# Kernel tuning notes

Hardware: AMD Instinct MI355X
Metric: run time of the kernel (lower is better)

## Reference

```python
import jax, jax.numpy as jnp
import numpy as np

NUM_LAYERS = 3
CHANNELS = 8
IN_CHANNELS = 8
MASK_OUT_STRIDE = 4
WEIGHT_NUMS = [(IN_CHANNELS + 2) * CHANNELS, CHANNELS * CHANNELS, CHANNELS]  # [80, 64, 8]
BIAS_NUMS = [CHANNELS, CHANNELS, 1]
NUM_GEN = sum(WEIGHT_NUMS) + sum(BIAS_NUMS)  # 169


def parse_params(params, weight_nums, bias_nums, channels):
    # params: [n_inst, sum(weight_nums)+sum(bias_nums)]
    n = params.shape[0]
    sizes = list(weight_nums) + list(bias_nums)
    splits = jnp.split(params, np.cumsum(sizes)[:-1].tolist(), axis=1)
    L = len(weight_nums)
    ws, bs = [], []
    for l in range(L):
        cout = channels if l < L - 1 else 1
        ws.append(splits[l].reshape(n, cout, -1))       # [n, cout, cin]
        bs.append(splits[L + l].reshape(n, cout))        # [n, cout]
    return ws, bs


def mask_head(x, ws, bs):
    # x: [n, cin, HW]; per-instance 1x1 convs == batched small GEMMs
    x_concat = None
    L = len(ws)
    for i, (w, b) in enumerate(zip(ws, bs)):
        x = jnp.einsum('noc,nch->noh', w, x) + b[:, :, None]
        if i < L - 1:
            x = jax.nn.relu(x)
        if i == L - 2:
            x_concat = x
    return x, x_concat


def aligned_bilinear(x, factor):
    # faithful port of AdelaiDet aligned_bilinear (align_corners=True interp)
    if factor == 1:
        return x
    n, c, h, w = x.shape
    x = jnp.pad(x, ((0, 0), (0, 0), (0, 1), (0, 1)), mode='edge')  # [h+1, w+1]
    oh, ow = factor * h + 1, factor * w + 1

    def interp_axis(arr, out_len, axis):
        # align_corners=True with out = factor*in - factor + 1 -> src = dst/factor exactly
        pos = jnp.arange(out_len) / factor
        i0 = jnp.floor(pos).astype(jnp.int32)
        i1 = jnp.minimum(i0 + 1, arr.shape[axis] - 1)
        frac = (pos - i0).astype(arr.dtype)
        a0 = jnp.take(arr, i0, axis=axis)
        a1 = jnp.take(arr, i1, axis=axis)
        shp = [1] * arr.ndim
        shp[axis] = out_len
        frac = frac.reshape(shp)
        return a0 * (1 - frac) + a1 * frac

    x = interp_axis(x, oh, 2)
    x = interp_axis(x, ow, 3)
    p = factor // 2
    x = jnp.pad(x, ((0, 0), (0, 0), (p, 0), (p, 0)), mode='edge')
    return x[:, :, :oh - 1, :ow - 1]


def setup_inputs() -> dict:
    key = jax.random.key(0)
    k1, k2, k3, k4, k5, k6 = jax.random.split(key, 6)
    N, Cin, H, W = 2, IN_CHANNELS, 100, 152
    n_inst = 128
    return {
        'mask_feats_body': jax.random.normal(k1, (N, Cin, H, W), dtype=jnp.float32),
        'mask_feats_edge': jax.random.normal(k2, (N, Cin, H, W), dtype=jnp.float32),
        'mask_head_params': jax.random.normal(k3, (n_inst, 2 * NUM_GEN + 81), dtype=jnp.float32) * 0.2,
        'inst_locations': jax.random.uniform(k4, (n_inst, 2), dtype=jnp.float32) * jnp.array([W * 8.0, H * 8.0]),
        'sizes_of_interest': jnp.array([64.0, 128.0, 256.0, 512.0, 1024.0], dtype=jnp.float32),
        'im_inds': jax.random.randint(k5, (n_inst,), 0, N, dtype=jnp.int32),
        'fpn_levels': jax.random.randint(k6, (n_inst,), 0, 5, dtype=jnp.int32),
        'mask_feat_stride': 8,
    }


def reference(mask_feats_body, mask_feats_edge, mask_head_params, inst_locations,
              sizes_of_interest, im_inds, fpn_levels, mask_feat_stride):
    N, Cin, H, W = mask_feats_body.shape
    n_inst = mask_head_params.shape[0]
    stride = mask_feat_stride

    # compute_locations: (x, y) grid at feature stride, offset stride//2
    shifts_x = jnp.arange(W, dtype=jnp.float32) * stride + stride // 2
    shifts_y = jnp.arange(H, dtype=jnp.float32) * stride + stride // 2
    sy, sx = jnp.meshgrid(shifts_y, shifts_x, indexing='ij')
    locations = jnp.stack([sx.reshape(-1), sy.reshape(-1)], axis=1)  # [HW, 2]

    rel = inst_locations[:, None, :] - locations[None, :, :]          # [n, HW, 2]
    rel = jnp.transpose(rel, (0, 2, 1))                               # [n, 2, HW]
    soi = sizes_of_interest[fpn_levels]                               # [n]
    rel = rel / soi[:, None, None]

    fb = mask_feats_body[im_inds].reshape(n_inst, Cin, H * W)
    fe = mask_feats_edge[im_inds].reshape(n_inst, Cin, H * W)
    inp_b = jnp.concatenate([rel, fb], axis=1)   # [n, Cin+2, HW]
    inp_e = jnp.concatenate([rel, fe], axis=1)

    wb, bb = parse_params(mask_head_params[:, :NUM_GEN], WEIGHT_NUMS, BIAS_NUMS, CHANNELS)
    we, be = parse_params(mask_head_params[:, NUM_GEN:2 * NUM_GEN], WEIGHT_NUMS, BIAS_NUMS, CHANNELS)
    wf, bf = parse_params(mask_head_params[:, 2 * NUM_GEN:], WEIGHT_NUMS[1:], BIAS_NUMS[1:], CHANNELS)

    logits_b, concat_b = mask_head(inp_b, wb, bb)
    logits_e, concat_e = mask_head(inp_e, we, be)
    logits_f, _ = mask_head(concat_b + concat_e, wf, bf)

    factor = mask_feat_stride // MASK_OUT_STRIDE
    outs = []
    for l in (logits_b, logits_e, logits_f):
        l = l.reshape(n_inst, 1, H, W)
        outs.append(jax.nn.sigmoid(aligned_bilinear(l, factor)))
    return tuple(outs)
```

## Files before the change

kernel.cpp:

```cpp
#include <hip/hip_runtime.h>
#include <hip/hip_bf16.h>
#include <hip/hip_fp16.h>

#define CIN      8
#define HH       100
#define WW       152
#define HWSZ     (HH * WW)
#define OHGT     200
#define OWID     304
#define PPI      419
#define OUT_PER_INST (OHGT * OWID)

#define RSTRIP   5
#define TROWS    6
#define NSTRIPS  20
#define QPT      38
#define P1THREADS (TROWS * QPT)
#define P2ITEMS  (3 * RSTRIP * 76)


typedef float vf4 __attribute__((ext_vector_type(4)));

__device__ __forceinline__ vf4 fma4(float w, vf4 x, vf4 a) { return w * x + a; }
__device__ __forceinline__ vf4 relu4(vf4 x) {
    vf4 r; r.x = fmaxf(x.x, 0.f); r.y = fmaxf(x.y, 0.f);
    r.z = fmaxf(x.z, 0.f); r.w = fmaxf(x.w, 0.f); return r;
}

__global__ __launch_bounds__(256, 4) void dmh_fused6_kernel(
    const float* __restrict__ fbody,
    const float* __restrict__ fedge,
    const float* __restrict__ params,
    const float* __restrict__ locs,
    const float* __restrict__ soi_tab,
    const int*   __restrict__ im_inds,
    const int*   __restrict__ fpn_levels,
    float* __restrict__ out,
    int n_inst)
{
    const int s   = blockIdx.x;
    const int n   = blockIdx.y;
    const int tid = threadIdx.x;
    const int r0  = RSTRIP * s;

    __shared__ float slog[3][TROWS][WW];

    const float* __restrict__ p = params + (size_t)n * PPI;
    const int   im      = im_inds[n];
    const float inv_soi = 1.0f / soi_tab[fpn_levels[n]];
    const float sx = (locs[2 * n]     - 4.0f) * inv_soi;
    const float sy = (locs[2 * n + 1] - 4.0f) * inv_soi;
    const float k8 = 8.0f * inv_soi;

    if (tid < P1THREADS) {
        const int rl = tid / QPT;
        const int c  = (tid - rl * QPT) * 4;
        const int r  = min(r0 + rl, HH - 1);
        const int px = r * WW + c;

        const float dx0 = sx - (float)c * k8;
        const vf4 dx = { dx0, dx0 - k8, dx0 - 2.f * k8, dx0 - 3.f * k8 };
        const float dyv = sy - (float)r * k8;
        const vf4 dy = { dyv, dyv, dyv, dyv };

        const float* __restrict__ fb = fbody + (size_t)im * CIN * HWSZ + px;
        const float* __restrict__ fe = fedge + (size_t)im * CIN * HWSZ + px;

        vf4 inb[10], ine[8];
        inb[0] = dx; inb[1] = dy;
        #pragma unroll
        for (int k = 0; k < 8; ++k)
            inb[k + 2] = *(const vf4*)(fb + k * HWSZ);
        #pragma unroll
        for (int k = 0; k < 8; ++k)
            ine[k] = *(const vf4*)(fe + k * HWSZ);

        vf4 h1[8];

        #pragma unroll
        for (int o = 0; o < 8; ++o) {
            vf4 a = p[152 + o];
            #pragma unroll
            for (int k = 0; k < 10; ++k) a = fma4(p[o * 10 + k], inb[k], a);
            h1[o] = relu4(a);
        }
        vf4 h2b[8];
        #pragma unroll
        for (int o = 0; o < 8; ++o) {
            vf4 a = p[160 + o];
            #pragma unroll
            for (int k = 0; k < 8; ++k) a = fma4(p[80 + o * 8 + k], h1[k], a);
            h2b[o] = relu4(a);
        }
        vf4 lb = p[168];
        #pragma unroll
        for (int k = 0; k < 8; ++k) lb = fma4(p[144 + k], h2b[k], lb);

        #pragma unroll
        for (int o = 0; o < 8; ++o) {
            vf4 a = p[169 + 152 + o];
            a = fma4(p[169 + o * 10 + 0], dx, a);
            a = fma4(p[169 + o * 10 + 1], dy, a);
            #pragma unroll
            for (int k = 0; k < 8; ++k) a = fma4(p[169 + o * 10 + 2 + k], ine[k], a);
            h1[o] = relu4(a);
        }
        vf4 le = p[169 + 168];
        #pragma unroll
        for (int o = 0; o < 8; ++o) {
            vf4 a = p[169 + 160 + o];
            #pragma unroll
            for (int k = 0; k < 8; ++k) a = fma4(p[169 + 80 + o * 8 + k], h1[k], a);
            const vf4 he = relu4(a);
            le = fma4(p[169 + 144 + o], he, le);
            h2b[o] = h2b[o] + he;
        }

        vf4 hf[8];
        #pragma unroll
        for (int o = 0; o < 8; ++o) {
            vf4 a = p[410 + o];
            #pragma unroll
            for (int k = 0; k < 8; ++k) a = fma4(p[338 + o * 8 + k], h2b[k], a);
            hf[o] = relu4(a);
        }
        vf4 lf = p[418];
        #pragma unroll
        for (int k = 0; k < 8; ++k) lf = fma4(p[402 + k], hf[k], lf);

        *(vf4*)&slog[0][rl][c] = lb;
        *(vf4*)&slog[1][rl][c] = le;
        *(vf4*)&slog[2][rl][c] = lf;
    }
    __syncthreads();

    for (int it = tid; it < P2ITEMS; it += 256) {
        const int h   = it / (RSTRIP * 76);
        const int rem = it - h * (RSTRIP * 76);
        const int rr  = rem / 76;
        const int q   = rem - rr * 76;
        const int r   = r0 + rr;

        const int cm = max(2 * q - 1, 0);
        const int c0 = 2 * q;
        const int cp = min(2 * q + 1, WW - 1);

        const float Lm0 = slog[h][rr][cm],     L00 = slog[h][rr][c0],     Lp0 = slog[h][rr][cp];
        const float Lm1 = slog[h][rr + 1][cm], L01 = slog[h][rr + 1][c0], Lp1 = slog[h][rr + 1][cp];

        const float a0 = 0.5f * (Lm0 + L00);
        const float a1 = L00;
        const float a2 = 0.5f * (L00 + Lp0);
        const float a3 = Lp0;
        const float m  = 0.5f * (Lm0 + Lm1);
        const float z  = 0.5f * (L00 + L01);
        const float pz = 0.5f * (Lp0 + Lp1);
        const float b0 = 0.5f * (m + z);
        const float b1 = z;
        const float b2 = 0.5f * (z + pz);
        const float b3 = pz;

        vf4 A, B;
        A.x = 1.0f / (1.0f + __expf(-a0));
        A.y = 1.0f / (1.0f + __expf(-a1));
        A.z = 1.0f / (1.0f + __expf(-a2));
        A.w = 1.0f / (1.0f + __expf(-a3));
        B.x = 1.0f / (1.0f + __expf(-b0));
        B.y = 1.0f / (1.0f + __expf(-b1));
        B.z = 1.0f / (1.0f + __expf(-b2));
        B.w = 1.0f / (1.0f + __expf(-b3));

        float* __restrict__ O = out + ((size_t)h * n_inst + n) * OUT_PER_INST;
        const int xq = 4 * q;
        __builtin_nontemporal_store(A, (vf4*)(O + (size_t)(2 * r + 1) * OWID + xq));
        if (r == 0)
            __builtin_nontemporal_store(A, (vf4*)(O + xq));
        if (r < HH - 1)
            __builtin_nontemporal_store(B, (vf4*)(O + (size_t)(2 * r + 2) * OWID + xq));
    }
}

extern "C" void kernel_launch(void* const* d_in, const int* in_sizes, int n_in,
                              void* d_out, int out_size, void* d_ws, size_t ws_size,
                              hipStream_t stream) {
    const float* fbody   = (const float*)d_in[0];
    const float* fedge   = (const float*)d_in[1];
    const float* params  = (const float*)d_in[2];
    const float* locs    = (const float*)d_in[3];
    const float* soi     = (const float*)d_in[4];
    const int*   im_inds = (const int*)d_in[5];
    const int*   fpn     = (const int*)d_in[6];

    const int n_inst = in_sizes[5];

    dim3 grid(NSTRIPS, n_inst);
    dmh_fused6_kernel<<<grid, dim3(256), 0, stream>>>(
        fbody, fedge, params, locs, soi, im_inds, fpn,
        (float*)d_out, n_inst);
}
```

Before: 42.87 us.

## Double strip height and process two pixel quads per thread in MLP phase

Strips grow from 5 to 10 output rows, halving the block count and the fraction of halo rows recomputed. Each thread now evaluates the three dynamic mask heads for two quads instead of one, sharing the scalar weight loads between them. The min-blocks launch bound is dropped. This raises register pressure and per-block latency and reduces parallelism, so lower occupancy may offset the saved halo work and weight loads.

```diff
diff --git a/kernel.cpp b/kernel.cpp
--- a/kernel.cpp
+++ b/kernel.cpp
@@ -11,11 +11,10 @@
 #define PPI      419
 #define OUT_PER_INST (OHGT * OWID)
 
-#define RSTRIP   5
-#define TROWS    6
-#define NSTRIPS  20
-#define QPT      38
-#define P1THREADS (TROWS * QPT)
+#define RSTRIP   10
+#define TROWS    11
+#define NSTRIPS  10
+#define NQUAD    (TROWS * 38)
 #define P2ITEMS  (3 * RSTRIP * 76)
 
 
@@ -27,7 +26,7 @@
     r.z = fmaxf(x.z, 0.f); r.w = fmaxf(x.w, 0.f); return r;
 }
 
-__global__ __launch_bounds__(256, 4) void dmh_fused6_kernel(
+__global__ __launch_bounds__(256) void dmh_fused7_kernel(
     const float* __restrict__ fbody,
     const float* __restrict__ fedge,
     const float* __restrict__ params,
@@ -52,85 +51,134 @@
     const float sy = (locs[2 * n + 1] - 4.0f) * inv_soi;
     const float k8 = 8.0f * inv_soi;
 
-    if (tid < P1THREADS) {
-        const int rl = tid / QPT;
-        const int c  = (tid - rl * QPT) * 4;
-        const int r  = min(r0 + rl, HH - 1);
-        const int px = r * WW + c;
-
-        const float dx0 = sx - (float)c * k8;
-        const vf4 dx = { dx0, dx0 - k8, dx0 - 2.f * k8, dx0 - 3.f * k8 };
-        const float dyv = sy - (float)r * k8;
-        const vf4 dy = { dyv, dyv, dyv, dyv };
-
-        const float* __restrict__ fb = fbody + (size_t)im * CIN * HWSZ + px;
-        const float* __restrict__ fe = fedge + (size_t)im * CIN * HWSZ + px;
-
-        vf4 inb[10], ine[8];
-        inb[0] = dx; inb[1] = dy;
-        #pragma unroll
-        for (int k = 0; k < 8; ++k)
-            inb[k + 2] = *(const vf4*)(fb + k * HWSZ);
-        #pragma unroll
-        for (int k = 0; k < 8; ++k)
-            ine[k] = *(const vf4*)(fe + k * HWSZ);
-
-        vf4 h1[8];
-
-        #pragma unroll
-        for (int o = 0; o < 8; ++o) {
-            vf4 a = p[152 + o];
-            #pragma unroll
-            for (int k = 0; k < 10; ++k) a = fma4(p[o * 10 + k], inb[k], a);
-            h1[o] = relu4(a);
-        }
-        vf4 h2b[8];
-        #pragma unroll
-        for (int o = 0; o < 8; ++o) {
-            vf4 a = p[160 + o];
-            #pragma unroll
-            for (int k = 0; k < 8; ++k) a = fma4(p[80 + o * 8 + k], h1[k], a);
-            h2b[o] = relu4(a);
-        }
-        vf4 lb = p[168];
-        #pragma unroll
-        for (int k = 0; k < 8; ++k) lb = fma4(p[144 + k], h2b[k], lb);
-
-        #pragma unroll
-        for (int o = 0; o < 8; ++o) {
-            vf4 a = p[169 + 152 + o];
-            a = fma4(p[169 + o * 10 + 0], dx, a);
-            a = fma4(p[169 + o * 10 + 1], dy, a);
-            #pragma unroll
-            for (int k = 0; k < 8; ++k) a = fma4(p[169 + o * 10 + 2 + k], ine[k], a);
-            h1[o] = relu4(a);
-        }
-        vf4 le = p[169 + 168];
-        #pragma unroll
-        for (int o = 0; o < 8; ++o) {
-            vf4 a = p[169 + 160 + o];
-            #pragma unroll
-            for (int k = 0; k < 8; ++k) a = fma4(p[169 + 80 + o * 8 + k], h1[k], a);
-            const vf4 he = relu4(a);
-            le = fma4(p[169 + 144 + o], he, le);
-            h2b[o] = h2b[o] + he;
-        }
-
-        vf4 hf[8];
-        #pragma unroll
-        for (int o = 0; o < 8; ++o) {
-            vf4 a = p[410 + o];
-            #pragma unroll
-            for (int k = 0; k < 8; ++k) a = fma4(p[338 + o * 8 + k], h2b[k], a);
-            hf[o] = relu4(a);
-        }
-        vf4 lf = p[418];
-        #pragma unroll
-        for (int k = 0; k < 8; ++k) lf = fma4(p[402 + k], hf[k], lf);
-
-        *(vf4*)&slog[0][rl][c] = lb;
-        *(vf4*)&slog[1][rl][c] = le;
-        *(vf4*)&slog[2][rl][c] = lf;
+    const float* __restrict__ fb_base = fbody + (size_t)im * CIN * HWSZ;
+    const float* __restrict__ fe_base = fedge + (size_t)im * CIN * HWSZ;
+
+    if (tid < 228) {
+        const bool hasB = (tid < NQUAD - 228);
+        const int qA = tid;
+        const int qB = hasB ? tid + 228 : tid;
+
+        const int rlA = qA / 38, cA = (qA - rlA * 38) * 4;
+        const int rlB = qB / 38, cB = (qB - rlB * 38) * 4;
+        const int rA = min(r0 + rlA, HH - 1);
+        const int rB = min(r0 + rlB, HH - 1);
+        const int pxA = rA * WW + cA;
+        const int pxB = rB * WW + cB;
+
+        const float dxA0 = sx - (float)cA * k8;
+        const float dxB0 = sx - (float)cB * k8;
+        const vf4 dxA = { dxA0, dxA0 - k8, dxA0 - 2.f * k8, dxA0 - 3.f * k8 };
+        const vf4 dxB = { dxB0, dxB0 - k8, dxB0 - 2.f * k8, dxB0 - 3.f * k8 };
+        const float dyAv = sy - (float)rA * k8;
+        const float dyBv = sy - (float)rB * k8;
+        const vf4 dyA = { dyAv, dyAv, dyAv, dyAv };
+        const vf4 dyB = { dyBv, dyBv, dyBv, dyBv };
+
+        vf4 fA[8], fB[8], gA[8], gB[8];
+        #pragma unroll
+        for (int k = 0; k < 8; ++k) {
+            fA[k] = *(const vf4*)(fb_base + k * HWSZ + pxA);
+            fB[k] = *(const vf4*)(fb_base + k * HWSZ + pxB);
+        }
+        #pragma unroll
+        for (int k = 0; k < 8; ++k) {
+            gA[k] = *(const vf4*)(fe_base + k * HWSZ + pxA);
+            gB[k] = *(const vf4*)(fe_base + k * HWSZ + pxB);
+        }
+
+        vf4 h1A[8], h1B[8];
+
+        #pragma unroll
+        for (int o = 0; o < 8; ++o) {
+            const float b = p[152 + o];
+            vf4 aA = b, aB = b;
+            const float w0 = p[o * 10 + 0], w1 = p[o * 10 + 1];
+            aA = fma4(w0, dxA, aA); aB = fma4(w0, dxB, aB);
+            aA = fma4(w1, dyA, aA); aB = fma4(w1, dyB, aB);
+            #pragma unroll
+            for (int k = 0; k < 8; ++k) {
+                const float w = p[o * 10 + 2 + k];
+                aA = fma4(w, fA[k], aA); aB = fma4(w, fB[k], aB);
+            }
+            h1A[o] = relu4(aA); h1B[o] = relu4(aB);
+        }
+        vf4 h2bA[8], h2bB[8];
+        #pragma unroll
+        for (int o = 0; o < 8; ++o) {
+            const float b = p[160 + o];
+            vf4 aA = b, aB = b;
+            #pragma unroll
+            for (int k = 0; k < 8; ++k) {
+                const float w = p[80 + o * 8 + k];
+                aA = fma4(w, h1A[k], aA); aB = fma4(w, h1B[k], aB);
+            }
+            h2bA[o] = relu4(aA); h2bB[o] = relu4(aB);
+        }
+        vf4 lbA = p[168], lbB = p[168];
+        #pragma unroll
+        for (int k = 0; k < 8; ++k) {
+            const float w = p[144 + k];
+            lbA = fma4(w, h2bA[k], lbA); lbB = fma4(w, h2bB[k], lbB);
+        }
+
+        #pragma unroll
+        for (int o = 0; o < 8; ++o) {
+            const float b = p[169 + 152 + o];
+            vf4 aA = b, aB = b;
+            const float w0 = p[169 + o * 10 + 0], w1 = p[169 + o * 10 + 1];
+            aA = fma4(w0, dxA, aA); aB = fma4(w0, dxB, aB);
+            aA = fma4(w1, dyA, aA); aB = fma4(w1, dyB, aB);
+            #pragma unroll
+            for (int k = 0; k < 8; ++k) {
+                const float w = p[169 + o * 10 + 2 + k];
+                aA = fma4(w, gA[k], aA); aB = fma4(w, gB[k], aB);
+            }
+            h1A[o] = relu4(aA); h1B[o] = relu4(aB);
+        }
+        vf4 leA = p[169 + 168], leB = p[169 + 168];
+        #pragma unroll
+        for (int o = 0; o < 8; ++o) {
+            const float b = p[169 + 160 + o];
+            vf4 aA = b, aB = b;
+            #pragma unroll
+            for (int k = 0; k < 8; ++k) {
+                const float w = p[169 + 80 + o * 8 + k];
+                aA = fma4(w, h1A[k], aA); aB = fma4(w, h1B[k], aB);
+            }
+            const vf4 heA = relu4(aA), heB = relu4(aB);
+            const float w3 = p[169 + 144 + o];
+            leA = fma4(w3, heA, leA); leB = fma4(w3, heB, leB);
+            h2bA[o] = h2bA[o] + heA; h2bB[o] = h2bB[o] + heB;
+        }
+
+        vf4 hfA[8], hfB[8];
+        #pragma unroll
+        for (int o = 0; o < 8; ++o) {
+            const float b = p[410 + o];
+            vf4 aA = b, aB = b;
+            #pragma unroll
+            for (int k = 0; k < 8; ++k) {
+                const float w = p[338 + o * 8 + k];
+                aA = fma4(w, h2bA[k], aA); aB = fma4(w, h2bB[k], aB);
+            }
+            hfA[o] = relu4(aA); hfB[o] = relu4(aB);
+        }
+        vf4 lfA = p[418], lfB = p[418];
+        #pragma unroll
+        for (int k = 0; k < 8; ++k) {
+            const float w = p[402 + k];
+            lfA = fma4(w, hfA[k], lfA); lfB = fma4(w, hfB[k], lfB);
+        }
+
+        *(vf4*)&slog[0][rlA][cA] = lbA;
+        *(vf4*)&slog[1][rlA][cA] = leA;
+        *(vf4*)&slog[2][rlA][cA] = lfA;
+        if (hasB) {
+            *(vf4*)&slog[0][rlB][cB] = lbB;
+            *(vf4*)&slog[1][rlB][cB] = leB;
+            *(vf4*)&slog[2][rlB][cB] = lfB;
+        }
     }
     __syncthreads();
 
@@ -194,7 +242,7 @@
     const int n_inst = in_sizes[5];
 
     dim3 grid(NSTRIPS, n_inst);
-    dmh_fused6_kernel<<<grid, dim3(256), 0, stream>>>(
+    dmh_fused7_kernel<<<grid, dim3(256), 0, stream>>>(
         fbody, fedge, params, locs, soi, im_inds, fpn,
         (float*)d_out, n_inst);
 }
```

Measured after the change: 62.54 us. 1.46x slower.
